# Performance work log

Hardware: AMD Instinct MI355X
Metric: run time of the kernel (lower is better)

Reference implementation:

```python
import jax, jax.numpy as jnp
import numpy as np

KS = 2            # kernel_size
NUM_SHARED = 3    # len(num_shared_channels)
NBR_PARAM = 3     # nbr_param_layers
COUT = 128        # num_shared_channels[-1] == num_inputs
NUM_INPUTS = 128
D_R = 320         # ts2vec_output_dims
GEN_LEN = NBR_PARAM * COUT * COUT * KS


def _causal_conv(x, w, b, d):
    # x: [N, Ci, T], w: [Co, Ci, K], b: [Co]; left-pad (K-1)*d == pad+chomp in torch
    N, Ci, T = x.shape
    K = w.shape[-1]
    pad = (K - 1) * d
    xp = jnp.pad(x, ((0, 0), (0, 0), (pad, 0)))
    out = jnp.zeros((N, w.shape[0], T), dtype=x.dtype)
    for k in range(K):  # K==2, tiny static loop
        out = out + jnp.einsum('oc,nct->not', w[:, :, k], xp[:, :, k * d:k * d + T])
    return out + b[None, :, None]


def _causal_conv_group(x, w, d):
    # groups=N conv with per-sample weights. x: [N, C, T], w: [N, Co, C, K], no bias
    N, C, T = x.shape
    K = w.shape[-1]
    pad = (K - 1) * d
    xp = jnp.pad(x, ((0, 0), (0, 0), (pad, 0)))
    out = jnp.zeros((N, w.shape[1], T), dtype=x.dtype)
    for k in range(K):
        out = out + jnp.einsum('noc,nct->not', w[..., k], xp[:, :, k * d:k * d + T])
    return out


def setup_inputs() -> dict:
    key = jax.random.key(0)
    ks = jax.random.split(key, 12)
    N, T = 16, 1024
    x = jax.random.normal(ks[0], (N, T, NUM_INPUTS), dtype=jnp.float32)
    r = jax.random.normal(ks[1], (N, D_R), dtype=jnp.float32)
    # shared TemporalBlock params (in==out==COUT, so no downsample conv)
    wscale = 1.0 / np.sqrt(COUT * KS)
    shared_w1 = wscale * jax.random.normal(ks[2], (NUM_SHARED, COUT, COUT, KS), dtype=jnp.float32)
    shared_b1 = 0.01 * jax.random.normal(ks[3], (NUM_SHARED, COUT), dtype=jnp.float32)
    shared_w2 = wscale * jax.random.normal(ks[4], (NUM_SHARED, COUT, COUT, KS), dtype=jnp.float32)
    shared_b2 = 0.01 * jax.random.normal(ks[5], (NUM_SHARED, COUT), dtype=jnp.float32)
    # hypernetwork (f_param_generator) + additive base weights (last_conv_layers)
    fparam_W = 0.01 * jax.random.normal(ks[6], (GEN_LEN, D_R), dtype=jnp.float32)
    fparam_b = 0.01 * jax.random.normal(ks[7], (GEN_LEN,), dtype=jnp.float32)
    last_bias = 0.001 * jax.random.normal(ks[8], (GEN_LEN,), dtype=jnp.float32) + 1.0 / (KS * COUT)
    # output head
    lin_W = (1.0 / np.sqrt(COUT)) * jax.random.normal(ks[9], (NUM_INPUTS, COUT), dtype=jnp.float32)
    lin_b = 0.01 * jax.random.normal(ks[10], (NUM_INPUTS,), dtype=jnp.float32)
    return {"x": x, "r": r, "f_out_same_in_size": 1,
            "shared_w1": shared_w1, "shared_b1": shared_b1,
            "shared_w2": shared_w2, "shared_b2": shared_b2,
            "fparam_W": fparam_W, "fparam_b": fparam_b, "last_bias": last_bias,
            "lin_W": lin_W, "lin_b": lin_b}


def reference(x, r, f_out_same_in_size, shared_w1, shared_b1, shared_w2, shared_b2,
              fparam_W, fparam_b, last_bias, lin_W, lin_b):
    N, T, _ = x.shape
    h = jnp.swapaxes(x, 1, 2)  # [N, C, T]
    # shared TemporalBlocks (dropout p=0 -> identity)
    for i in range(NUM_SHARED):
        d = 2 ** i
        res = h
        a = jax.nn.relu(_causal_conv(h, shared_w1[i], shared_b1[i], d))
        a = jax.nn.relu(_causal_conv(a, shared_w2[i], shared_b2[i], d))
        h = jax.nn.relu(a + res)
    # hypernet-generated per-sample grouped conv layers
    gen = r @ fparam_W.T + fparam_b + last_bias           # [N, GEN_LEN]
    allw = gen.reshape(NBR_PARAM, N, COUT, COUT, KS)      # same layout as torch .view
    for i in range(NBR_PARAM):
        d = 2 ** (NUM_SHARED + i)
        res = h
        c = _causal_conv_group(h, allw[i], d)
        h = jax.nn.relu(jax.nn.relu(c) + res)             # relu(dropout(relu(c)) + res), p=0
    out = jnp.einsum('nct,oc->nto', h, lin_W) + lin_b     # [N, T, NUM_INPUTS]
    if not f_out_same_in_size:
        out = out[:, -1, :]
    return out
```

## Files before the change

### kernel.cpp

```cpp
#include <hip/hip_runtime.h>

#define NB    16
#define TLEN  1024
#define CCH   128
#define DR    320

typedef _Float16 h8 __attribute__((ext_vector_type(8)));
typedef _Float16 h4 __attribute__((ext_vector_type(4)));
typedef _Float16 h2 __attribute__((ext_vector_type(2)));
typedef float    f4 __attribute__((ext_vector_type(4)));

__device__ __forceinline__ void gload16h(const _Float16* g, _Float16* l) {
  __builtin_amdgcn_global_load_lds(
      (const __attribute__((address_space(1))) void*)g,
      (__attribute__((address_space(3))) void*)l, 16, 0, 0);
}
__device__ __forceinline__ void gload16f(const float* g, float* l) {
  __builtin_amdgcn_global_load_lds(
      (const __attribute__((address_space(1))) void*)g,
      (__attribute__((address_space(3))) void*)l, 16, 0, 0);
}

__global__ __launch_bounds__(256) void k_init(const float* __restrict__ x,
                                              const float* __restrict__ w1,
                                              const float* __restrict__ w2,
                                              const float* __restrict__ linw,
                                              const float* __restrict__ fb,
                                              const float* __restrict__ lb,
                                              _Float16* __restrict__ h0,
                                              _Float16* __restrict__ Wsh,
                                              _Float16* __restrict__ linWh,
                                              float* __restrict__ fblb2) {
  int i = blockIdx.x * 256 + threadIdx.x;
  const float4* src = (const float4*)x + (size_t)i * 2;
  float4 a = src[0], b = src[1];
  h8 v;
  v[0] = (_Float16)a.x; v[1] = (_Float16)a.y; v[2] = (_Float16)a.z; v[3] = (_Float16)a.w;
  v[4] = (_Float16)b.x; v[5] = (_Float16)b.y; v[6] = (_Float16)b.z; v[7] = (_Float16)b.w;
  *(h8*)(h0 + (size_t)i * 8) = v;

  if (i < 6 * 32768) {
    int c = i & 127, k = (i >> 7) & 1, o = (i >> 8) & 127, i3 = i >> 15;
    const float* srcw = (i3 < 3) ? (w1 + i3 * 32768) : (w2 + (i3 - 3) * 32768);
    Wsh[i] = (_Float16)srcw[(o * 128 + c) * 2 + k];
  }
  if (i < 16384) linWh[i] = (_Float16)linw[i];
  if (i < 98304) fblb2[i] = fb[i] + lb[i];
}

__global__ __launch_bounds__(256) void k_gen4(const float* __restrict__ r,
                                              const float* __restrict__ fW,
                                              const float* __restrict__ fblb2,
                                              _Float16* __restrict__ wg) {
  __shared__ alignas(16) float buf[3][32 * DR];
  __shared__ alignas(16) float csc[4][16][16];
  __shared__ alignas(16) float fbl[384];
  const int tid = threadIdx.x;
  const size_t rbase = (size_t)blockIdx.x * 384;

  const int l = tid & 63, w = tid >> 6;
  const int l15 = l & 15, lh = l >> 4;
  const int rt = w >> 1, kh = w & 1;

  f4 rx[5], ry[5];
  const float* rp = r + l15 * DR + kh * 160 + lh * 8;
#pragma unroll
  for (int cb = 0; cb < 5; cb++) {
    rx[cb] = *(const f4*)(rp + cb * 32);
    ry[cb] = *(const f4*)(rp + cb * 32 + 4);
  }
  if (tid < 96) gload16f(fblb2 + rbase + tid * 4, fbl + tid * 4);
#pragma unroll
  for (int t = 0; t < 3; t++) {
    const float* s = fW + (rbase + (size_t)t * 32) * DR;
#pragma unroll
    for (int i = 0; i < 10; i++) {
      int f = tid + i * 256;
      gload16f(s + (size_t)f * 4, (float*)buf[t] + (size_t)f * 4);
    }
  }
  h8 bfr[5];
#pragma unroll
  for (int cb = 0; cb < 5; cb++) {
    h8 v;
    v[0] = (_Float16)rx[cb][0]; v[1] = (_Float16)rx[cb][1];
    v[2] = (_Float16)rx[cb][2]; v[3] = (_Float16)rx[cb][3];
    v[4] = (_Float16)ry[cb][0]; v[5] = (_Float16)ry[cb][1];
    v[6] = (_Float16)ry[cb][2]; v[7] = (_Float16)ry[cb][3];
    bfr[cb] = v;
  }
  asm volatile("s_waitcnt vmcnt(20) lgkmcnt(0)" ::: "memory");
  __builtin_amdgcn_s_barrier();
  __builtin_amdgcn_sched_barrier(0);

  const int rn = tid >> 4, rk = (tid >> 3) & 1, rcq = tid & 7;

  for (int j = 0; j < 12; j++) {
    const float* bp = (const float*)buf[j % 3];
    f4 acc = {0.f, 0.f, 0.f, 0.f};
    const float* arow = bp + (rt * 16 + l15) * DR + kh * 160 + lh * 8;
#pragma unroll
    for (int cb = 0; cb < 5; cb++) {
      f4 x = *(const f4*)(arow + cb * 32);
      f4 y = *(const f4*)(arow + cb * 32 + 4);
      h8 a;
      a[0] = (_Float16)x[0]; a[1] = (_Float16)x[1];
      a[2] = (_Float16)x[2]; a[3] = (_Float16)x[3];
      a[4] = (_Float16)y[0]; a[5] = (_Float16)y[1];
      a[6] = (_Float16)y[2]; a[7] = (_Float16)y[3];
      acc = __builtin_amdgcn_mfma_f32_16x16x32_f16(a, bfr[cb], acc, 0, 0, 0);
    }
#pragma unroll
    for (int rr = 0; rr < 4; rr++) csc[w][lh * 4 + rr][l15] = acc[rr];

    asm volatile("s_waitcnt lgkmcnt(0)" ::: "memory");
    __builtin_amdgcn_s_barrier();
    __builtin_amdgcn_sched_barrier(0);

    {
      const unsigned g32 = (unsigned)(rbase + (size_t)j * 32);
      const unsigned G = g32 >> 15, o = (g32 >> 8) & 127u, c0 = (g32 & 255u) >> 1;
      h2 v2;
#pragma unroll
      for (int i = 0; i < 2; i++) {
        int rl32 = (rcq * 2 + i) * 2 + rk;
        int hp = (rl32 >> 4) * 2, rr2 = rl32 & 15;
        float s = csc[hp][rr2][rn] + csc[hp + 1][rr2][rn] + fbl[j * 32 + rl32];
        v2[i] = (_Float16)s;
      }
      unsigned q = 3u * (unsigned)rn + G;
      *(h2*)&wg[(((size_t)q * 128 + o) * 2 + rk) * 128 + c0 + rcq * 2] = v2;
    }

    if (j <= 8) {
      float* dstb = (float*)buf[j % 3];
      const float* src = fW + (rbase + (size_t)(j + 3) * 32) * DR;
#pragma unroll
      for (int i = 0; i < 10; i++) {
        int f = tid + i * 256;
        gload16f(src + (size_t)f * 4, dstb + (size_t)f * 4);
      }
    }

    if (j < 10)
      asm volatile("s_waitcnt vmcnt(11) lgkmcnt(0)" ::: "memory");
    else if (j == 10)
      asm volatile("s_waitcnt vmcnt(2) lgkmcnt(0)" ::: "memory");
    else
      asm volatile("s_waitcnt vmcnt(0) lgkmcnt(0)" ::: "memory");
    __builtin_amdgcn_s_barrier();
    __builtin_amdgcn_sched_barrier(0);
  }
}

template <int D>
__global__ __launch_bounds__(256) void k_pair(const _Float16* __restrict__ in,
                                              _Float16* __restrict__ out,
                                              const _Float16* __restrict__ w1p,
                                              const _Float16* __restrict__ w2p,
                                              const float* __restrict__ b1p,
                                              const float* __restrict__ b2p) {
  constexpr int HA = 16;
  constexpr int HI = HA + D;
  constexpr int RIN = 80 + D;
  __shared__ _Float16 hin_l[RIN * 128];
  __shared__ _Float16 a_l[80 * 128];

  const int tid = threadIdx.x;
  const int n = blockIdx.y, t0 = blockIdx.x * 64;
  const _Float16* inN = in + (size_t)n * (TLEN * CCH);

  if (blockIdx.x == 0) {
    for (int f = tid; f < HI * 16; f += 256)
      *(int4*)(hin_l + (size_t)f * 8) = make_int4(0, 0, 0, 0);
    for (int f = HI * 16 + tid; f < RIN * 16; f += 256) {
      int p = f >> 4, l16 = f & 15;
      int c8 = (l16 ^ (p & 15)) << 3;
      gload16h(inN + (t0 - HI + p) * 128 + c8, hin_l + f * 8);
    }
  } else {
    for (int f = tid; f < RIN * 16; f += 256) {
      int p = f >> 4, l16 = f & 15;
      int c8 = (l16 ^ (p & 15)) << 3;
      gload16h(inN + (t0 - HI + p) * 128 + c8, hin_l + f * 8);
    }
  }
  __syncthreads();

  const int l = tid & 63, w = tid >> 6;
  const int l15 = l & 15, lh = l >> 4;
  const int o0 = w * 32;

  f4 acc1[2][5] = {};
#pragma unroll
  for (int tap = 0; tap < 2; tap++) {
#pragma unroll
    for (int cb = 0; cb < 4; cb++) {
      const int c0 = cb * 32 + lh * 8;
      h8 a[2], bfr[5];
#pragma unroll
      for (int i2 = 0; i2 < 2; i2++) {
        int o = o0 + i2 * 16 + l15;
        a[i2] = *(const h8*)&w1p[(o * 2 + tap) * 128 + c0];
      }
#pragma unroll
      for (int jt = 0; jt < 5; jt++) {
        int p = jt * 16 + l15 + tap * D;
        int cs = c0 ^ ((p & 15) << 3);
        bfr[jt] = *(const h8*)&hin_l[p * 128 + cs];
      }
#pragma unroll
      for (int i2 = 0; i2 < 2; i2++)
#pragma unroll
        for (int jt = 0; jt < 5; jt++)
          acc1[i2][jt] = __builtin_amdgcn_mfma_f32_16x16x32_f16(
              a[i2], bfr[jt], acc1[i2][jt], 0, 0, 0);
    }
  }
#pragma unroll
  for (int i2 = 0; i2 < 2; i2++) {
    f4 bv = *(const f4*)&b1p[o0 + i2 * 16 + lh * 4];
    const int base8 = o0 + i2 * 16 + (lh >> 1) * 8;
    const int sub = (lh & 1) * 4;
#pragma unroll
    for (int jt = 0; jt < 5; jt++) {
      int p = jt * 16 + l15;
      h4 sv;
      if (blockIdx.x == 0 && jt == 0) {
        sv[0] = sv[1] = sv[2] = sv[3] = (_Float16)0.f;
      } else {
        f4 v = acc1[i2][jt];
#pragma unroll
        for (int rr = 0; rr < 4; rr++) sv[rr] = (_Float16)fmaxf(v[rr] + bv[rr], 0.f);
      }
      *(h4*)&a_l[p * 128 + (base8 ^ ((p & 15) << 3)) + sub] = sv;
    }
  }
  __syncthreads();

  f4 acc2[2][4] = {};
#pragma unroll
  for (int tap = 0; tap < 2; tap++) {
#pragma unroll
    for (int cb = 0; cb < 4; cb++) {
      const int c0 = cb * 32 + lh * 8;
      h8 a[2], bfr[4];
#pragma unroll
      for (int i2 = 0; i2 < 2; i2++) {
        int o = o0 + i2 * 16 + l15;
        a[i2] = *(const h8*)&w2p[(o * 2 + tap) * 128 + c0];
      }
#pragma unroll
      for (int jt = 0; jt < 4; jt++) {
        int pa = jt * 16 + l15 + (HA - D) + tap * D;
        int cs = c0 ^ ((pa & 15) << 3);
        bfr[jt] = *(const h8*)&a_l[pa * 128 + cs];
      }
#pragma unroll
      for (int i2 = 0; i2 < 2; i2++)
#pragma unroll
        for (int jt = 0; jt < 4; jt++)
          acc2[i2][jt] = __builtin_amdgcn_mfma_f32_16x16x32_f16(
              a[i2], bfr[jt], acc2[i2][jt], 0, 0, 0);
    }
  }

  _Float16* outN = out + (size_t)n * (TLEN * CCH);
#pragma unroll
  for (int i2 = 0; i2 < 2; i2++) {
    f4 bv = *(const f4*)&b2p[o0 + i2 * 16 + lh * 4];
    const int base8 = o0 + i2 * 16 + (lh >> 1) * 8;
    const int sub = (lh & 1) * 4;
#pragma unroll
    for (int jt = 0; jt < 4; jt++) {
      int t = t0 + jt * 16 + l15;
      int pr = jt * 16 + l15 + HA + D;
      h4 rv = *(const h4*)&hin_l[pr * 128 + (base8 ^ ((pr & 15) << 3)) + sub];
      f4 v = acc2[i2][jt];
      h4 sv;
#pragma unroll
      for (int rr = 0; rr < 4; rr++) {
        float z = fmaxf(v[rr] + bv[rr], 0.f);
        sv[rr] = (_Float16)fmaxf(z + (float)rv[rr], 0.f);
      }
      *(h4*)&outN[t * 128 + o0 + i2 * 16 + lh * 4] = sv;
    }
  }
}

template <int D>
__global__ __launch_bounds__(256) void k_gconv(const _Float16* __restrict__ in,
                                               _Float16* __restrict__ out,
                                               const _Float16* __restrict__ wBase) {
  __shared__ _Float16 Wl[256 * 128];
  __shared__ _Float16 hl[(64 + D) * 128];
  const int tid = threadIdx.x;
  const int n = blockIdx.y, t0 = blockIdx.x * 64;
  const _Float16* inN = in + (size_t)n * (TLEN * CCH);
  const _Float16* wp = wBase + (size_t)n * 32768;

  for (int f = tid; f < 4096; f += 256) {
    int row = f >> 4, l16 = f & 15;
    int c8 = (l16 ^ ((row >> 1) & 15)) << 3;
    gload16h(wp + row * 128 + c8, Wl + f * 8);
  }
  if (blockIdx.x == 0) {
    for (int f = tid; f < D * 16; f += 256)
      *(int4*)(hl + (size_t)f * 8) = make_int4(0, 0, 0, 0);
    for (int f = D * 16 + tid; f < (64 + D) * 16; f += 256) {
      int p = f >> 4, l16 = f & 15;
      int c8 = (l16 ^ (p & 15)) << 3;
      gload16h(inN + (t0 - D + p) * 128 + c8, hl + f * 8);
    }
  } else {
    for (int f = tid; f < (64 + D) * 16; f += 256) {
      int p = f >> 4, l16 = f & 15;
      int c8 = (l16 ^ (p & 15)) << 3;
      gload16h(inN + (t0 - D + p) * 128 + c8, hl + f * 8);
    }
  }
  __syncthreads();

  const int l = tid & 63, w = tid >> 6;
  const int l15 = l & 15, lh = l >> 4;
  const int o0 = w * 32;
  f4 acc[2][4] = {};

#pragma unroll
  for (int tap = 0; tap < 2; tap++) {
#pragma unroll
    for (int cb = 0; cb < 4; cb++) {
      const int c0 = cb * 32 + 8 * lh;
      h8 a[2], bfr[4];
#pragma unroll
      for (int i2 = 0; i2 < 2; i2++) {
        int o = o0 + i2 * 16 + l15;
        int cs = c0 ^ ((o & 15) << 3);
        a[i2] = *(const h8*)&Wl[(o * 2 + tap) * 128 + cs];
      }
#pragma unroll
      for (int jt = 0; jt < 4; jt++) {
        int p = jt * 16 + l15 + tap * D;
        int cs = c0 ^ ((p & 15) << 3);
        bfr[jt] = *(const h8*)&hl[p * 128 + cs];
      }
#pragma unroll
      for (int i2 = 0; i2 < 2; i2++)
#pragma unroll
        for (int jt = 0; jt < 4; jt++)
          acc[i2][jt] = __builtin_amdgcn_mfma_f32_16x16x32_f16(
              a[i2], bfr[jt], acc[i2][jt], 0, 0, 0);
    }
  }

  _Float16* outN = out + (size_t)n * (TLEN * CCH);
#pragma unroll
  for (int i2 = 0; i2 < 2; i2++) {
    const int base8 = o0 + i2 * 16 + (lh >> 1) * 8;
    const int sub = (lh & 1) * 4;
#pragma unroll
    for (int jt = 0; jt < 4; jt++) {
      int t = t0 + jt * 16 + l15;
      int pr = jt * 16 + l15 + D;
      h4 rv = *(const h4*)&hl[pr * 128 + (base8 ^ ((pr & 15) << 3)) + sub];
      f4 v = acc[i2][jt];
      h4 sv;
#pragma unroll
      for (int rr = 0; rr < 4; rr++) {
        float z = fmaxf(v[rr], 0.f);
        sv[rr] = (_Float16)fmaxf(z + (float)rv[rr], 0.f);
      }
      *(h4*)&outN[t * 128 + o0 + i2 * 16 + lh * 4] = sv;
    }
  }
}

__global__ __launch_bounds__(256) void k_glin(const _Float16* __restrict__ in,
                                              float* __restrict__ outp,
                                              const _Float16* __restrict__ wBase,
                                              const _Float16* __restrict__ linWh,
                                              const float* __restrict__ lbias) {
  constexpr int D = 32;
  __shared__ _Float16 Wl[256 * 128];
  __shared__ _Float16 hl[(64 + D) * 128];
  __shared__ _Float16 a_l[64 * 128];
  const int tid = threadIdx.x;
  const int n = blockIdx.y, t0 = blockIdx.x * 64;
  const _Float16* inN = in + (size_t)n * (TLEN * CCH);
  const _Float16* wp = wBase + (size_t)n * 32768;

  for (int f = tid; f < 4096; f += 256) {
    int row = f >> 4, l16 = f & 15;
    int c8 = (l16 ^ ((row >> 1) & 15)) << 3;
    gload16h(wp + row * 128 + c8, Wl + f * 8);
  }
  if (blockIdx.x == 0) {
    for (int f = tid; f < D * 16; f += 256)
      *(int4*)(hl + (size_t)f * 8) = make_int4(0, 0, 0, 0);
    for (int f = D * 16 + tid; f < (64 + D) * 16; f += 256) {
      int p = f >> 4, l16 = f & 15;
      int c8 = (l16 ^ (p & 15)) << 3;
      gload16h(inN + (t0 - D + p) * 128 + c8, hl + f * 8);
    }
  } else {
    for (int f = tid; f < (64 + D) * 16; f += 256) {
      int p = f >> 4, l16 = f & 15;
      int c8 = (l16 ^ (p & 15)) << 3;
      gload16h(inN + (t0 - D + p) * 128 + c8, hl + f * 8);
    }
  }
  __syncthreads();

  const int l = tid & 63, w = tid >> 6;
  const int l15 = l & 15, lh = l >> 4;
  const int o0 = w * 32;
  f4 acc[2][4] = {};

#pragma unroll
  for (int tap = 0; tap < 2; tap++) {
#pragma unroll
    for (int cb = 0; cb < 4; cb++) {
      const int c0 = cb * 32 + 8 * lh;
      h8 a[2], bfr[4];
#pragma unroll
      for (int i2 = 0; i2 < 2; i2++) {
        int o = o0 + i2 * 16 + l15;
        int cs = c0 ^ ((o & 15) << 3);
        a[i2] = *(const h8*)&Wl[(o * 2 + tap) * 128 + cs];
      }
#pragma unroll
      for (int jt = 0; jt < 4; jt++) {
        int p = jt * 16 + l15 + tap * D;
        int cs = c0 ^ ((p & 15) << 3);
        bfr[jt] = *(const h8*)&hl[p * 128 + cs];
      }
#pragma unroll
      for (int i2 = 0; i2 < 2; i2++)
#pragma unroll
        for (int jt = 0; jt < 4; jt++)
          acc[i2][jt] = __builtin_amdgcn_mfma_f32_16x16x32_f16(
              a[i2], bfr[jt], acc[i2][jt], 0, 0, 0);
    }
  }

#pragma unroll
  for (int i2 = 0; i2 < 2; i2++) {
    const int base8 = o0 + i2 * 16 + (lh >> 1) * 8;
    const int sub = (lh & 1) * 4;
#pragma unroll
    for (int jt = 0; jt < 4; jt++) {
      int p = jt * 16 + l15;
      int pr = p + D;
      h4 rv = *(const h4*)&hl[pr * 128 + (base8 ^ ((pr & 15) << 3)) + sub];
      f4 v = acc[i2][jt];
      h4 sv;
#pragma unroll
      for (int rr = 0; rr < 4; rr++) {
        float z = fmaxf(v[rr], 0.f);
        sv[rr] = (_Float16)fmaxf(z + (float)rv[rr], 0.f);
      }
      *(h4*)&a_l[p * 128 + (base8 ^ (l15 << 3)) + sub] = sv;
    }
  }
  __syncthreads();

  f4 acc3[2][4] = {};
#pragma unroll
  for (int cb = 0; cb < 4; cb++) {
    const int c0 = cb * 32 + lh * 8;
    h8 a[2], bfr[4];
#pragma unroll
    for (int i2 = 0; i2 < 2; i2++) {
      int o = o0 + i2 * 16 + l15;
      a[i2] = *(const h8*)&linWh[o * 128 + c0];
    }
#pragma unroll
    for (int jt = 0; jt < 4; jt++) {
      int p = jt * 16 + l15;
      int cs = c0 ^ ((p & 15) << 3);
      bfr[jt] = *(const h8*)&a_l[p * 128 + cs];
    }
#pragma unroll
    for (int i2 = 0; i2 < 2; i2++)
#pragma unroll
      for (int jt = 0; jt < 4; jt++)
        acc3[i2][jt] = __builtin_amdgcn_mfma_f32_16x16x32_f16(
            a[i2], bfr[jt], acc3[i2][jt], 0, 0, 0);
  }

#pragma unroll
  for (int i2 = 0; i2 < 2; i2++) {
    int o = o0 + i2 * 16 + lh * 4;
    f4 bv = *(const f4*)&lbias[o];
#pragma unroll
    for (int jt = 0; jt < 4; jt++) {
      int t = t0 + jt * 16 + l15;
      f4 v = acc3[i2][jt];
      float4 sv = make_float4(v[0] + bv[0], v[1] + bv[1], v[2] + bv[2], v[3] + bv[3]);
      *(float4*)&outp[((size_t)n * TLEN + t) * CCH + o] = sv;
    }
  }
}

extern "C" void kernel_launch(void* const* d_in, const int* in_sizes, int n_in,
                              void* d_out, int out_size, void* d_ws, size_t ws_size,
                              hipStream_t stream) {
  const float* x  = (const float*)d_in[0];
  const float* r  = (const float*)d_in[1];
  const float* w1 = (const float*)d_in[3];
  const float* b1 = (const float*)d_in[4];
  const float* w2 = (const float*)d_in[5];
  const float* b2 = (const float*)d_in[6];
  const float* fW = (const float*)d_in[7];
  const float* fb = (const float*)d_in[8];
  const float* lb = (const float*)d_in[9];
  const float* lw = (const float*)d_in[10];
  const float* lbias = (const float*)d_in[11];
  float* out = (float*)d_out;

  _Float16* h0    = (_Float16*)d_ws;
  _Float16* h1    = h0 + 2097152;
  _Float16* Wsh   = h1 + 2097152;
  _Float16* linWh = Wsh + 393216;
  _Float16* Wg    = linWh + 16384;
  float*    fblb2 = (float*)(Wg + 1572864);

  k_init<<<1024, 256, 0, stream>>>(x, w1, w2, lw, fb, lb, h0, Wsh, linWh, fblb2);
  k_gen4<<<256, 256, 0, stream>>>(r, fW, fblb2, Wg);

  const dim3 cg(16, 16);
  k_pair<1><<<cg, 256, 0, stream>>>(h0, h1, Wsh + 0 * 32768, Wsh + 3 * 32768,
                                    b1, b2);
  k_pair<2><<<cg, 256, 0, stream>>>(h1, h0, Wsh + 1 * 32768, Wsh + 4 * 32768,
                                    b1 + 128, b2 + 128);
  k_pair<4><<<cg, 256, 0, stream>>>(h0, h1, Wsh + 2 * 32768, Wsh + 5 * 32768,
                                    b1 + 256, b2 + 256);
  k_gconv<8> <<<cg, 256, 0, stream>>>(h1, h0, Wg);
  k_gconv<16><<<cg, 256, 0, stream>>>(h0, h1, Wg + 524288);
  k_glin<<<cg, 256, 0, stream>>>(h1, out, Wg + 1048576, linWh, lbias);
}
```

Before: 82.63 us.

## Fuse hypernet weight generation with first shared temporal block launch

Merges the hypernetwork weight-generation kernel and the first TemporalBlock kernel into one launch. Blocks 0-191 run generation and blocks 192-447 run pair<1>, using a shared-memory union. Each generation block now handles 512 rows instead of 384, and the load-wait counts are reworked for the longer pipeline. The two independent jobs can now overlap on the GPU and one launch gap is removed. In exchange, launch_bounds(256,1) and the large union LDS footprint may lower occupancy for the pair blocks.

```diff
diff --git a/kernel.cpp b/kernel.cpp
--- a/kernel.cpp
+++ b/kernel.cpp
@@ -48,15 +48,24 @@
   if (i < 98304) fblb2[i] = fb[i] + lb[i];
 }
 
-__global__ __launch_bounds__(256) void k_gen4(const float* __restrict__ r,
-                                              const float* __restrict__ fW,
-                                              const float* __restrict__ fblb2,
-                                              _Float16* __restrict__ wg) {
-  __shared__ alignas(16) float buf[3][32 * DR];
-  __shared__ alignas(16) float csc[4][16][16];
-  __shared__ alignas(16) float fbl[384];
-  const int tid = threadIdx.x;
-  const size_t rbase = (size_t)blockIdx.x * 384;
+struct SGen {
+  float buf[3][32 * DR];
+  float csc[4][16][16];
+  float fbl[512];
+};
+struct SPair {
+  _Float16 hin[84 * 128];
+  _Float16 a[80 * 128];
+};
+union alignas(16) SU { SGen g; SPair p; };
+
+__device__ __forceinline__ void gen_body(SGen& S, int bid, int tid,
+                                         const float* __restrict__ r,
+                                         const float* __restrict__ fW,
+                                         const float* __restrict__ fblb2,
+                                         _Float16* __restrict__ wg) {
+  constexpr int NT = 16;
+  const size_t rbase = (size_t)bid * 512;
 
   const int l = tid & 63, w = tid >> 6;
   const int l15 = l & 15, lh = l >> 4;
@@ -69,14 +78,14 @@
     rx[cb] = *(const f4*)(rp + cb * 32);
     ry[cb] = *(const f4*)(rp + cb * 32 + 4);
   }
-  if (tid < 96) gload16f(fblb2 + rbase + tid * 4, fbl + tid * 4);
+  if (tid < 128) gload16f(fblb2 + rbase + tid * 4, S.fbl + tid * 4);
 #pragma unroll
   for (int t = 0; t < 3; t++) {
     const float* s = fW + (rbase + (size_t)t * 32) * DR;
 #pragma unroll
     for (int i = 0; i < 10; i++) {
       int f = tid + i * 256;
-      gload16f(s + (size_t)f * 4, (float*)buf[t] + (size_t)f * 4);
+      gload16f(s + (size_t)f * 4, (float*)S.buf[t] + (size_t)f * 4);
     }
   }
   h8 bfr[5];
@@ -95,8 +104,8 @@
 
   const int rn = tid >> 4, rk = (tid >> 3) & 1, rcq = tid & 7;
 
-  for (int j = 0; j < 12; j++) {
-    const float* bp = (const float*)buf[j % 3];
+  for (int j = 0; j < NT; j++) {
+    const float* bp = (const float*)S.buf[j % 3];
     f4 acc = {0.f, 0.f, 0.f, 0.f};
     const float* arow = bp + (rt * 16 + l15) * DR + kh * 160 + lh * 8;
 #pragma unroll
@@ -111,7 +120,7 @@
       acc = __builtin_amdgcn_mfma_f32_16x16x32_f16(a, bfr[cb], acc, 0, 0, 0);
     }
 #pragma unroll
-    for (int rr = 0; rr < 4; rr++) csc[w][lh * 4 + rr][l15] = acc[rr];
+    for (int rr = 0; rr < 4; rr++) S.csc[w][lh * 4 + rr][l15] = acc[rr];
 
     asm volatile("s_waitcnt lgkmcnt(0)" ::: "memory");
     __builtin_amdgcn_s_barrier();
@@ -125,15 +134,16 @@
       for (int i = 0; i < 2; i++) {
         int rl32 = (rcq * 2 + i) * 2 + rk;
         int hp = (rl32 >> 4) * 2, rr2 = rl32 & 15;
-        float s = csc[hp][rr2][rn] + csc[hp + 1][rr2][rn] + fbl[j * 32 + rl32];
+        float s = S.csc[hp][rr2][rn] + S.csc[hp + 1][rr2][rn] + S.fbl[j * 32 + rl32];
         v2[i] = (_Float16)s;
       }
       unsigned q = 3u * (unsigned)rn + G;
       *(h2*)&wg[(((size_t)q * 128 + o) * 2 + rk) * 128 + c0 + rcq * 2] = v2;
     }
-
-    if (j <= 8) {
-      float* dstb = (float*)buf[j % 3];
+    __builtin_amdgcn_sched_barrier(0);
+
+    if (j + 3 < NT) {
+      float* dstb = (float*)S.buf[j % 3];
       const float* src = fW + (rbase + (size_t)(j + 3) * 32) * DR;
 #pragma unroll
       for (int i = 0; i < 10; i++) {
@@ -142,14 +152,163 @@
       }
     }
 
-    if (j < 10)
-      asm volatile("s_waitcnt vmcnt(11) lgkmcnt(0)" ::: "memory");
-    else if (j == 10)
-      asm volatile("s_waitcnt vmcnt(2) lgkmcnt(0)" ::: "memory");
+    if (j + 4 <= NT)
+      asm volatile("s_waitcnt vmcnt(20) lgkmcnt(0)" ::: "memory");
+    else if (j + 3 == NT)
+      asm volatile("s_waitcnt vmcnt(10) lgkmcnt(0)" ::: "memory");
     else
       asm volatile("s_waitcnt vmcnt(0) lgkmcnt(0)" ::: "memory");
     __builtin_amdgcn_s_barrier();
     __builtin_amdgcn_sched_barrier(0);
+  }
+}
+
+template <int D>
+__device__ __forceinline__ void pair_body(SPair& S, int tx, int n, int tid,
+                                          const _Float16* in, _Float16* out,
+                                          const _Float16* w1p, const _Float16* w2p,
+                                          const float* b1p, const float* b2p) {
+  constexpr int HA = 16;
+  constexpr int HI = HA + D;
+  constexpr int RIN = 80 + D;
+  static_assert(RIN * 128 <= sizeof(SPair::hin) / sizeof(_Float16), "hin size");
+  _Float16* hin_l = S.hin;
+  _Float16* a_l = S.a;
+  const int t0 = tx * 64;
+  const _Float16* inN = in + (size_t)n * (TLEN * CCH);
+
+  if (tx == 0) {
+    for (int f = tid; f < HI * 16; f += 256)
+      *(int4*)(hin_l + (size_t)f * 8) = make_int4(0, 0, 0, 0);
+    for (int f = HI * 16 + tid; f < RIN * 16; f += 256) {
+      int p = f >> 4, l16 = f & 15;
+      int c8 = (l16 ^ (p & 15)) << 3;
+      gload16h(inN + (t0 - HI + p) * 128 + c8, hin_l + f * 8);
+    }
+  } else {
+    for (int f = tid; f < RIN * 16; f += 256) {
+      int p = f >> 4, l16 = f & 15;
+      int c8 = (l16 ^ (p & 15)) << 3;
+      gload16h(inN + (t0 - HI + p) * 128 + c8, hin_l + f * 8);
+    }
+  }
+  __syncthreads();
+
+  const int l = tid & 63, w = tid >> 6;
+  const int l15 = l & 15, lh = l >> 4;
+  const int o0 = w * 32;
+
+  f4 acc1[2][5] = {};
+#pragma unroll
+  for (int tap = 0; tap < 2; tap++) {
+#pragma unroll
+    for (int cb = 0; cb < 4; cb++) {
+      const int c0 = cb * 32 + lh * 8;
+      h8 a[2], bfr[5];
+#pragma unroll
+      for (int i2 = 0; i2 < 2; i2++) {
+        int o = o0 + i2 * 16 + l15;
+        a[i2] = *(const h8*)&w1p[(o * 2 + tap) * 128 + c0];
+      }
+#pragma unroll
+      for (int jt = 0; jt < 5; jt++) {
+        int p = jt * 16 + l15 + tap * D;
+        int cs = c0 ^ ((p & 15) << 3);
+        bfr[jt] = *(const h8*)&hin_l[p * 128 + cs];
+      }
+#pragma unroll
+      for (int i2 = 0; i2 < 2; i2++)
+#pragma unroll
+        for (int jt = 0; jt < 5; jt++)
+          acc1[i2][jt] = __builtin_amdgcn_mfma_f32_16x16x32_f16(
+              a[i2], bfr[jt], acc1[i2][jt], 0, 0, 0);
+    }
+  }
+#pragma unroll
+  for (int i2 = 0; i2 < 2; i2++) {
+    f4 bv = *(const f4*)&b1p[o0 + i2 * 16 + lh * 4];
+    const int base8 = o0 + i2 * 16 + (lh >> 1) * 8;
+    const int sub = (lh & 1) * 4;
+#pragma unroll
+    for (int jt = 0; jt < 5; jt++) {
+      int p = jt * 16 + l15;
+      h4 sv;
+      if (tx == 0 && jt == 0) {
+        sv[0] = sv[1] = sv[2] = sv[3] = (_Float16)0.f;
+      } else {
+        f4 v = acc1[i2][jt];
+#pragma unroll
+        for (int rr = 0; rr < 4; rr++) sv[rr] = (_Float16)fmaxf(v[rr] + bv[rr], 0.f);
+      }
+      *(h4*)&a_l[p * 128 + (base8 ^ ((p & 15) << 3)) + sub] = sv;
+    }
+  }
+  __syncthreads();
+
+  f4 acc2[2][4] = {};
+#pragma unroll
+  for (int tap = 0; tap < 2; tap++) {
+#pragma unroll
+    for (int cb = 0; cb < 4; cb++) {
+      const int c0 = cb * 32 + lh * 8;
+      h8 a[2], bfr[4];
+#pragma unroll
+      for (int i2 = 0; i2 < 2; i2++) {
+        int o = o0 + i2 * 16 + l15;
+        a[i2] = *(const h8*)&w2p[(o * 2 + tap) * 128 + c0];
+      }
+#pragma unroll
+      for (int jt = 0; jt < 4; jt++) {
+        int pa = jt * 16 + l15 + (HA - D) + tap * D;
+        int cs = c0 ^ ((pa & 15) << 3);
+        bfr[jt] = *(const h8*)&a_l[pa * 128 + cs];
+      }
+#pragma unroll
+      for (int i2 = 0; i2 < 2; i2++)
+#pragma unroll
+        for (int jt = 0; jt < 4; jt++)
+          acc2[i2][jt] = __builtin_amdgcn_mfma_f32_16x16x32_f16(
+              a[i2], bfr[jt], acc2[i2][jt], 0, 0, 0);
+    }
+  }
+
+  _Float16* outN = out + (size_t)n * (TLEN * CCH);
+#pragma unroll
+  for (int i2 = 0; i2 < 2; i2++) {
+    f4 bv = *(const f4*)&b2p[o0 + i2 * 16 + lh * 4];
+    const int base8 = o0 + i2 * 16 + (lh >> 1) * 8;
+    const int sub = (lh & 1) * 4;
+#pragma unroll
+    for (int jt = 0; jt < 4; jt++) {
+      int t = t0 + jt * 16 + l15;
+      int pr = jt * 16 + l15 + HA + D;
+      h4 rv = *(const h4*)&hin_l[pr * 128 + (base8 ^ ((pr & 15) << 3)) + sub];
+      f4 v = acc2[i2][jt];
+      h4 sv;
+#pragma unroll
+      for (int rr = 0; rr < 4; rr++) {
+        float z = fmaxf(v[rr] + bv[rr], 0.f);
+        sv[rr] = (_Float16)fmaxf(z + (float)rv[rr], 0.f);
+      }
+      *(h4*)&outN[t * 128 + o0 + i2 * 16 + lh * 4] = sv;
+    }
+  }
+}
+
+__global__ __launch_bounds__(256, 1) void k_genpair(
+    const float* __restrict__ r, const float* __restrict__ fW,
+    const float* __restrict__ fblb2, _Float16* __restrict__ wg,
+    const _Float16* __restrict__ h0, _Float16* __restrict__ h1,
+    const _Float16* __restrict__ Wsh,
+    const float* __restrict__ b1, const float* __restrict__ b2) {
+  __shared__ SU su;
+  const int bid = blockIdx.x, tid = threadIdx.x;
+  if (bid < 192) {
+    gen_body(su.g, bid, tid, r, fW, fblb2, wg);
+  } else {
+    int q = bid - 192;
+    pair_body<1>(su.p, q & 15, q >> 4, tid, h0, h1,
+                 Wsh, Wsh + 3 * 32768, b1, b2);
   }
 }
 
@@ -160,132 +319,9 @@
                                               const _Float16* __restrict__ w2p,
                                               const float* __restrict__ b1p,
                                               const float* __restrict__ b2p) {
-  constexpr int HA = 16;
-  constexpr int HI = HA + D;
-  constexpr int RIN = 80 + D;
-  __shared__ _Float16 hin_l[RIN * 128];
-  __shared__ _Float16 a_l[80 * 128];
-
-  const int tid = threadIdx.x;
-  const int n = blockIdx.y, t0 = blockIdx.x * 64;
-  const _Float16* inN = in + (size_t)n * (TLEN * CCH);
-
-  if (blockIdx.x == 0) {
-    for (int f = tid; f < HI * 16; f += 256)
-      *(int4*)(hin_l + (size_t)f * 8) = make_int4(0, 0, 0, 0);
-    for (int f = HI * 16 + tid; f < RIN * 16; f += 256) {
-      int p = f >> 4, l16 = f & 15;
-      int c8 = (l16 ^ (p & 15)) << 3;
-      gload16h(inN + (t0 - HI + p) * 128 + c8, hin_l + f * 8);
-    }
-  } else {
-    for (int f = tid; f < RIN * 16; f += 256) {
-      int p = f >> 4, l16 = f & 15;
-      int c8 = (l16 ^ (p & 15)) << 3;
-      gload16h(inN + (t0 - HI + p) * 128 + c8, hin_l + f * 8);
-    }
-  }
-  __syncthreads();
-
-  const int l = tid & 63, w = tid >> 6;
-  const int l15 = l & 15, lh = l >> 4;
-  const int o0 = w * 32;
-
-  f4 acc1[2][5] = {};
-#pragma unroll
-  for (int tap = 0; tap < 2; tap++) {
-#pragma unroll
-    for (int cb = 0; cb < 4; cb++) {
-      const int c0 = cb * 32 + lh * 8;
-      h8 a[2], bfr[5];
-#pragma unroll
-      for (int i2 = 0; i2 < 2; i2++) {
-        int o = o0 + i2 * 16 + l15;
-        a[i2] = *(const h8*)&w1p[(o * 2 + tap) * 128 + c0];
-      }
-#pragma unroll
-      for (int jt = 0; jt < 5; jt++) {
-        int p = jt * 16 + l15 + tap * D;
-        int cs = c0 ^ ((p & 15) << 3);
-        bfr[jt] = *(const h8*)&hin_l[p * 128 + cs];
-      }
-#pragma unroll
-      for (int i2 = 0; i2 < 2; i2++)
-#pragma unroll
-        for (int jt = 0; jt < 5; jt++)
-          acc1[i2][jt] = __builtin_amdgcn_mfma_f32_16x16x32_f16(
-              a[i2], bfr[jt], acc1[i2][jt], 0, 0, 0);
-    }
-  }
-#pragma unroll
-  for (int i2 = 0; i2 < 2; i2++) {
-    f4 bv = *(const f4*)&b1p[o0 + i2 * 16 + lh * 4];
-    const int base8 = o0 + i2 * 16 + (lh >> 1) * 8;
-    const int sub = (lh & 1) * 4;
-#pragma unroll
-    for (int jt = 0; jt < 5; jt++) {
-      int p = jt * 16 + l15;
-      h4 sv;
-      if (blockIdx.x == 0 && jt == 0) {
-        sv[0] = sv[1] = sv[2] = sv[3] = (_Float16)0.f;
-      } else {
-        f4 v = acc1[i2][jt];
-#pragma unroll
-        for (int rr = 0; rr < 4; rr++) sv[rr] = (_Float16)fmaxf(v[rr] + bv[rr], 0.f);
-      }
-      *(h4*)&a_l[p * 128 + (base8 ^ ((p & 15) << 3)) + sub] = sv;
-    }
-  }
-  __syncthreads();
-
-  f4 acc2[2][4] = {};
-#pragma unroll
-  for (int tap = 0; tap < 2; tap++) {
-#pragma unroll
-    for (int cb = 0; cb < 4; cb++) {
-      const int c0 = cb * 32 + lh * 8;
-      h8 a[2], bfr[4];
-#pragma unroll
-      for (int i2 = 0; i2 < 2; i2++) {
-        int o = o0 + i2 * 16 + l15;
-        a[i2] = *(const h8*)&w2p[(o * 2 + tap) * 128 + c0];
-      }
-#pragma unroll
-      for (int jt = 0; jt < 4; jt++) {
-        int pa = jt * 16 + l15 + (HA - D) + tap * D;
-        int cs = c0 ^ ((pa & 15) << 3);
-        bfr[jt] = *(const h8*)&a_l[pa * 128 + cs];
-      }
-#pragma unroll
-      for (int i2 = 0; i2 < 2; i2++)
-#pragma unroll
-        for (int jt = 0; jt < 4; jt++)
-          acc2[i2][jt] = __builtin_amdgcn_mfma_f32_16x16x32_f16(
-              a[i2], bfr[jt], acc2[i2][jt], 0, 0, 0);
-    }
-  }
-
-  _Float16* outN = out + (size_t)n * (TLEN * CCH);
-#pragma unroll
-  for (int i2 = 0; i2 < 2; i2++) {
-    f4 bv = *(const f4*)&b2p[o0 + i2 * 16 + lh * 4];
-    const int base8 = o0 + i2 * 16 + (lh >> 1) * 8;
-    const int sub = (lh & 1) * 4;
-#pragma unroll
-    for (int jt = 0; jt < 4; jt++) {
-      int t = t0 + jt * 16 + l15;
-      int pr = jt * 16 + l15 + HA + D;
-      h4 rv = *(const h4*)&hin_l[pr * 128 + (base8 ^ ((pr & 15) << 3)) + sub];
-      f4 v = acc2[i2][jt];
-      h4 sv;
-#pragma unroll
-      for (int rr = 0; rr < 4; rr++) {
-        float z = fmaxf(v[rr] + bv[rr], 0.f);
-        sv[rr] = (_Float16)fmaxf(z + (float)rv[rr], 0.f);
-      }
-      *(h4*)&outN[t * 128 + o0 + i2 * 16 + lh * 4] = sv;
-    }
-  }
+  __shared__ SPair sp;
+  pair_body<D>(sp, blockIdx.x, blockIdx.y, threadIdx.x, in, out, w1p, w2p,
+               b1p, b2p);
 }
 
 template <int D>
@@ -526,11 +562,9 @@
   float*    fblb2 = (float*)(Wg + 1572864);
 
   k_init<<<1024, 256, 0, stream>>>(x, w1, w2, lw, fb, lb, h0, Wsh, linWh, fblb2);
-  k_gen4<<<256, 256, 0, stream>>>(r, fW, fblb2, Wg);
+  k_genpair<<<448, 256, 0, stream>>>(r, fW, fblb2, Wg, h0, h1, Wsh, b1, b2);
 
   const dim3 cg(16, 16);
-  k_pair<1><<<cg, 256, 0, stream>>>(h0, h1, Wsh + 0 * 32768, Wsh + 3 * 32768,
-                                    b1, b2);
   k_pair<2><<<cg, 256, 0, stream>>>(h1, h0, Wsh + 1 * 32768, Wsh + 4 * 32768,
                                     b1 + 128, b2 + 128);
   k_pair<4><<<cg, 256, 0, stream>>>(h0, h1, Wsh + 2 * 32768, Wsh + 5 * 32768,
```

New measurement: 78.04 us. -5.5%, faster.
